# Kernel optimization log

Hardware: AMD Instinct MI355X
Metric: run time of the kernel (lower is better)

## Reference

```python
import jax, jax.numpy as jnp
from jax import lax
import numpy as np

B, C, H, W, D = 8, 128, 96, 96, 4  # D must equal 64//16 = 4 (one UAG per depth slice)


def setup_inputs() -> dict:
    key = jax.random.key(0)
    ks = jax.random.split(key, 9)
    s = 0.5 / np.sqrt(C)  # keep the recurrence numerically stable
    def w(k):
        return jax.random.normal(k, (D, C, C), jnp.float32) * s
    def b(k):
        return jax.random.normal(k, (D, C), jnp.float32) * 0.01
    return {
        "x": jax.random.normal(ks[0], (B, C, H, W, D), jnp.float32),
        "W1": w(ks[1]), "b1": b(ks[2]),  # conv1 per-dag weights/bias (kernel_size=1 -> [C,C])
        "W2": w(ks[3]), "b2": b(ks[4]),  # conv2
        "W4": w(ks[5]), "b4": b(ks[6]),  # conv4
        "W5": w(ks[7]), "b5": b(ks[8]),  # conv5
    }


def _dag(xs, w1, bb1, w2, bb2, w4, bb4, w5, bb5):
    # xs: [B,C,H,W]; one UAG_RNN_4Neigh forward.
    def lin(w, bb, v):  # 1x1 Conv1d == channel matmul; v: [B,C,L]
        return jnp.einsum('oc,bcl->bol', w, v) + bb[None, :, None]

    # --- row recurrence (top -> bottom); row 0 passes through unchanged ---
    def row_step(prev, row):
        new = jax.nn.relu(lin(w1, bb1, row) + lin(w2, bb2, prev))
        return new, new

    row0 = xs[:, :, 0, :]                       # [B,C,W]
    rows = jnp.moveaxis(xs[:, :, 1:, :], 2, 0)  # [H-1,B,C,W]
    _, out_rows = lax.scan(row_step, row0, rows)
    hs = jnp.concatenate([row0[None], out_rows], axis=0)  # [H,B,C,W]
    hs = jnp.moveaxis(hs, 0, 2)                            # [B,C,H,W]

    # --- col recurrence (left -> right); col 0 gets relu only ---
    def col_step(prev, col):
        new = jax.nn.relu(lin(w4, bb4, col) + lin(w5, bb5, prev))
        return new, new

    col0 = jax.nn.relu(hs[:, :, :, 0])           # [B,C,H]
    cols = jnp.moveaxis(hs[:, :, :, 1:], 3, 0)   # [W-1,B,C,H]
    _, out_cols = lax.scan(col_step, col0, cols)
    hse = jnp.concatenate([col0[None], out_cols], axis=0)  # [W,B,C,H]
    return jnp.moveaxis(hse, 0, 3)                           # [B,C,H,W]


def reference(x, W1, b1, W2, b2, W4, b4, W5, b5):
    # vmap over the D=4 depth slices, each with its own dag parameters
    hid = jax.vmap(_dag, in_axes=(-1, 0, 0, 0, 0, 0, 0, 0, 0), out_axes=-1)(
        x, W1, b1, W2, b2, W4, b4, W5, b5)
    return x + hid
```

## Files before the change

kernel.cpp:

```cpp
#include <hip/hip_runtime.h>


typedef short bf16x8 __attribute__((ext_vector_type(8)));
typedef float f32x4 __attribute__((ext_vector_type(4)));
typedef unsigned int uint4v __attribute__((ext_vector_type(4)));

__device__ __forceinline__ unsigned short f2bf(float f) {
  unsigned int u = __builtin_bit_cast(unsigned int, f);
  u = (u + 0x7FFFu + ((u >> 16) & 1u)) >> 16;
  return (unsigned short)u;
}
__device__ __forceinline__ float bf2f(unsigned short h) {
  unsigned int u = ((unsigned int)h) << 16;
  return __builtin_bit_cast(float, u);
}

__device__ __forceinline__ int sigma_k(int kap) {
  int kt = kap >> 5, q = (kap >> 3) & 3, j = kap & 7;
  return kt * 32 + ((j >> 2) << 4) + q * 4 + (j & 3);
}

__global__ __launch_bounds__(256) void prep_kernel(
    const float* __restrict__ W1, const float* __restrict__ b1,
    const float* __restrict__ W2, const float* __restrict__ b2,
    const float* __restrict__ W4, const float* __restrict__ b4,
    const float* __restrict__ W5, const float* __restrict__ b5,
    unsigned short* __restrict__ Wb, float* __restrict__ bs12,
    float* __restrict__ bs45) {
  int gid = blockIdx.x * 256 + threadIdx.x;
  if (gid < 4 * 65536) {
    int m = gid >> 16;
    int r = gid & 65535;
    int kap = r & 127;
    int c = sigma_k(kap);
    const float* src = (m == 0) ? W1 : (m == 1) ? W2 : (m == 2) ? W4 : W5;
    Wb[m * 65536 + r] = f2bf(src[(r >> 7) * 128 + c]);
  } else if (gid < 4 * 65536 + 512) {
    int r = gid - 4 * 65536;
    bs12[r] = b1[r] + b2[r];
  } else if (gid < 4 * 65536 + 1024) {
    int r = gid - 4 * 65536 - 512;
    bs45[r] = b4[r] + b5[r];
  }
}

__global__ __launch_bounds__(256) void transpose_kernel(
    const float* __restrict__ x, unsigned short* __restrict__ act) {
  __shared__ unsigned short tile[128 * 208];
  int bid = blockIdx.x;
  int half = bid & 1;
  int rest = bid >> 1;
  int h = rest % 96;
  int b = rest / 96;
  int wd0 = half * 192;
  int tid = threadIdx.x;
#pragma unroll
  for (int it = 0; it < 12; ++it) {
    int cid = it * 256 + tid;
    int c = cid / 24;
    int k = cid % 24;
    const float* xp = x + ((size_t)(b * 128 + c) * 96 + h) * 384 + wd0 + k * 8;
    float4 v0 = *(const float4*)xp;
    float4 v1 = *(const float4*)(xp + 4);
    bf16x8 pk;
    pk[0] = (short)f2bf(v0.x); pk[1] = (short)f2bf(v0.y);
    pk[2] = (short)f2bf(v0.z); pk[3] = (short)f2bf(v0.w);
    pk[4] = (short)f2bf(v1.x); pk[5] = (short)f2bf(v1.y);
    pk[6] = (short)f2bf(v1.z); pk[7] = (short)f2bf(v1.w);
    int ks = k ^ ((c >> 3) & 7);
    *(bf16x8*)&tile[c * 208 + ks * 8] = pk;
  }
  __syncthreads();
#pragma unroll
  for (int it = 0; it < 12; ++it) {
    int sid = it * 256 + tid;
    int wdl = sid >> 4;
    int cc = sid & 15;
    int k = wdl >> 3, off = wdl & 7;
    int ktq = cc >> 2, qq = cc & 3;
    bf16x8 pk;
#pragma unroll
    for (int j = 0; j < 8; ++j) {
      int c = ktq * 32 + ((j >> 2) << 4) + qq * 4 + (j & 3);
      int ks = k ^ ((c >> 3) & 7);
      pk[j] = (short)tile[c * 208 + ks * 8 + off];
    }
    int wdg = wd0 + wdl;
    int d = wdg & 3, w = wdg >> 2;
    *(bf16x8*)(act + ((((size_t)(b * 4 + d) * 96 + h) * 96 + w) * 128 + cc * 8)) = pk;
  }
}

__global__ __launch_bounds__(128) void row_kernel(
    unsigned short* act, const unsigned short* __restrict__ Wb,
    const float* __restrict__ bs12) {
  __shared__ float slots[4][8][64][4];
  __shared__ int flags[64];
  int bid = blockIdx.x;
  int wt = bid % 6;
  int bd = bid / 6;
  int d = bd & 3;
  int w0 = wt * 16;
  int tid = threadIdx.x;
  int wave = tid >> 6;
  int lane = tid & 63;
  int q = lane >> 4;
  int n = lane & 15;
  volatile int* fprod = &flags[0];
  volatile int* fcons = &flags[32];
  if (tid < 2) flags[tid * 32] = 0;
  __syncthreads();

  size_t bd9216 = (size_t)bd * 9216;
  size_t base = (bd9216 + (size_t)(w0 + n)) * 128 + q * 8;

  if (wave == 1) {
    const unsigned short* w1p = Wb + d * 16384;
    bf16x8 A1[8][4];
#pragma unroll
    for (int mi = 0; mi < 8; ++mi) {
      int c = mi * 16 + n;
#pragma unroll
      for (int kt = 0; kt < 4; ++kt)
        A1[mi][kt] = *(const bf16x8*)(w1p + c * 128 + kt * 32 + q * 8);
    }
    f32x4 bias[8];
#pragma unroll
    for (int mi = 0; mi < 8; ++mi)
#pragma unroll
      for (int r = 0; r < 4; ++r)
        bias[mi][r] = bs12[d * 128 + mi * 16 + q * 4 + r];
    const unsigned short* xrow = act + base;
    bf16x8 Bn[4], Bf[4];
#pragma unroll
    for (int kt = 0; kt < 4; ++kt) {
      Bn[kt] = *(const bf16x8*)(xrow + (size_t)1 * 12288 + kt * 32);
      Bf[kt] = *(const bf16x8*)(xrow + (size_t)2 * 12288 + kt * 32);
    }
#pragma unroll 1
    for (int h = 1; h <= 95; ++h) {
      while (h - *fcons > 3) __builtin_amdgcn_s_sleep(1);
      asm volatile("" ::: "memory");
      f32x4 acc[8];
#pragma unroll
      for (int mi = 0; mi < 8; ++mi)
        acc[mi] = __builtin_amdgcn_mfma_f32_16x16x32_bf16(A1[mi][0], Bn[0],
                                                          bias[mi], 0, 0, 0);
#pragma unroll
      for (int kt = 1; kt < 4; ++kt)
#pragma unroll
        for (int mi = 0; mi < 8; ++mi)
          acc[mi] = __builtin_amdgcn_mfma_f32_16x16x32_bf16(A1[mi][kt], Bn[kt],
                                                            acc[mi], 0, 0, 0);
      int hp = (h + 2 <= 95) ? h + 2 : 95;
      const unsigned short* pf = xrow + (size_t)hp * 12288;
#pragma unroll
      for (int kt = 0; kt < 4; ++kt) {
        Bn[kt] = Bf[kt];
        Bf[kt] = *(const bf16x8*)(pf + kt * 32);
      }
      float* sp = &slots[h & 3][0][lane][0];
#pragma unroll
      for (int mi = 0; mi < 8; ++mi)
        *(f32x4*)(sp + mi * 256) = acc[mi];
      asm volatile("s_waitcnt lgkmcnt(0)" ::: "memory");
      if (lane == 0) *fprod = h;
    }
  } else {
    const unsigned short* w2p = Wb + 65536 + d * 16384;
    bf16x8 A2[8][4];
#pragma unroll
    for (int mi = 0; mi < 8; ++mi) {
      int c = mi * 16 + n;
#pragma unroll
      for (int kt = 0; kt < 4; ++kt)
        A2[mi][kt] = *(const bf16x8*)(w2p + c * 128 + kt * 32 + q * 8);
    }
    const unsigned short* xrow = act + base;
    unsigned short* outrow = act + base + 12288;
    bf16x8 Bp[4];
#pragma unroll
    for (int kt = 0; kt < 4; ++kt)
      Bp[kt] = *(const bf16x8*)(xrow + kt * 32);
#pragma unroll 1
    for (int h = 1; h <= 95; ++h) {
      while (*fprod < h) __builtin_amdgcn_s_sleep(1);
      asm volatile("" ::: "memory");
      const float* sp = &slots[h & 3][0][lane][0];
      f32x4 acc[8];
#pragma unroll
      for (int mi = 0; mi < 8; ++mi)
        acc[mi] = *(const f32x4*)(sp + mi * 256);
#pragma unroll
      for (int kt = 0; kt < 4; ++kt)
#pragma unroll
        for (int mi = 0; mi < 8; ++mi)
          acc[mi] = __builtin_amdgcn_mfma_f32_16x16x32_bf16(A2[mi][kt], Bp[kt],
                                                            acc[mi], 0, 0, 0);
#pragma unroll
      for (int kt = 0; kt < 4; ++kt) {
        unsigned int u0, u1, u2, u3;
        float a0 = fmaxf(acc[2 * kt][0], 0.f);
        float a1 = fmaxf(acc[2 * kt][1], 0.f);
        float a2 = fmaxf(acc[2 * kt][2], 0.f);
        float a3 = fmaxf(acc[2 * kt][3], 0.f);
        float c0 = fmaxf(acc[2 * kt + 1][0], 0.f);
        float c1 = fmaxf(acc[2 * kt + 1][1], 0.f);
        float c2 = fmaxf(acc[2 * kt + 1][2], 0.f);
        float c3 = fmaxf(acc[2 * kt + 1][3], 0.f);
        asm("v_cvt_pk_bf16_f32 %0, %1, %2" : "=v"(u0) : "v"(a0), "v"(a1));
        asm("v_cvt_pk_bf16_f32 %0, %1, %2" : "=v"(u1) : "v"(a2), "v"(a3));
        asm("v_cvt_pk_bf16_f32 %0, %1, %2" : "=v"(u2) : "v"(c0), "v"(c1));
        asm("v_cvt_pk_bf16_f32 %0, %1, %2" : "=v"(u3) : "v"(c2), "v"(c3));
        uint4v uu;
        uu[0] = u0; uu[1] = u1; uu[2] = u2; uu[3] = u3;
        Bp[kt] = __builtin_bit_cast(bf16x8, uu);
        *(bf16x8*)(outrow + kt * 32) = Bp[kt];
      }
      outrow += 12288;
      asm volatile("" ::: "memory");
      if (lane == 0) *fcons = h;
    }
  }
}

__global__ __launch_bounds__(128) void col_kernel(
    unsigned short* act, const unsigned short* __restrict__ Wb,
    const float* __restrict__ bs45) {
  __shared__ float slots[4][8][64][4];
  __shared__ int flags[64];
  int bid = blockIdx.x;
  int ht = bid % 6;
  int bd = bid / 6;
  int d = bd & 3;
  int h0 = ht * 16;
  int tid = threadIdx.x;
  int wave = tid >> 6;
  int lane = tid & 63;
  int q = lane >> 4;
  int n = lane & 15;
  volatile int* fprod = &flags[0];
  volatile int* fcons = &flags[32];
  if (tid < 2) flags[tid * 32] = 0;
  __syncthreads();

  size_t bd9216 = (size_t)bd * 9216;
  size_t base = (bd9216 + (size_t)(h0 + n) * 96) * 128 + q * 8;

  if (wave == 1) {
    const unsigned short* w4p = Wb + 2 * 65536 + d * 16384;
    bf16x8 A1[8][4];
#pragma unroll
    for (int mi = 0; mi < 8; ++mi) {
      int c = mi * 16 + n;
#pragma unroll
      for (int kt = 0; kt < 4; ++kt)
        A1[mi][kt] = *(const bf16x8*)(w4p + c * 128 + kt * 32 + q * 8);
    }
    f32x4 bias[8];
#pragma unroll
    for (int mi = 0; mi < 8; ++mi)
#pragma unroll
      for (int r = 0; r < 4; ++r)
        bias[mi][r] = bs45[d * 128 + mi * 16 + q * 4 + r];
    const unsigned short* ccol = act + base;
    bf16x8 Bn[4], Bf[4];
#pragma unroll
    for (int kt = 0; kt < 4; ++kt) {
      Bn[kt] = *(const bf16x8*)(ccol + (size_t)1 * 128 + kt * 32);
      Bf[kt] = *(const bf16x8*)(ccol + (size_t)2 * 128 + kt * 32);
    }
#pragma unroll 1
    for (int w = 1; w <= 95; ++w) {
      while (w - *fcons > 3) __builtin_amdgcn_s_sleep(1);
      asm volatile("" ::: "memory");
      f32x4 acc[8];
#pragma unroll
      for (int mi = 0; mi < 8; ++mi)
        acc[mi] = __builtin_amdgcn_mfma_f32_16x16x32_bf16(A1[mi][0], Bn[0],
                                                          bias[mi], 0, 0, 0);
#pragma unroll
      for (int kt = 1; kt < 4; ++kt)
#pragma unroll
        for (int mi = 0; mi < 8; ++mi)
          acc[mi] = __builtin_amdgcn_mfma_f32_16x16x32_bf16(A1[mi][kt], Bn[kt],
                                                            acc[mi], 0, 0, 0);
      int wp = (w + 2 <= 95) ? w + 2 : 95;
      const unsigned short* pf = ccol + (size_t)wp * 128;
#pragma unroll
      for (int kt = 0; kt < 4; ++kt) {
        Bn[kt] = Bf[kt];
        Bf[kt] = *(const bf16x8*)(pf + kt * 32);
      }
      float* sp = &slots[w & 3][0][lane][0];
#pragma unroll
      for (int mi = 0; mi < 8; ++mi)
        *(f32x4*)(sp + mi * 256) = acc[mi];
      asm volatile("s_waitcnt lgkmcnt(0)" ::: "memory");
      if (lane == 0) *fprod = w;
    }
  } else {
    const unsigned short* w5p = Wb + 3 * 65536 + d * 16384;
    bf16x8 A2[8][4];
#pragma unroll
    for (int mi = 0; mi < 8; ++mi) {
      int c = mi * 16 + n;
#pragma unroll
      for (int kt = 0; kt < 4; ++kt)
        A2[mi][kt] = *(const bf16x8*)(w5p + c * 128 + kt * 32 + q * 8);
    }
    const unsigned short* ccol = act + base;
    unsigned short* outrow = act + base;
    bf16x8 Bp[4];
#pragma unroll
    for (int kt = 0; kt < 4; ++kt) {
      bf16x8 v = *(const bf16x8*)(ccol + kt * 32);
#pragma unroll
      for (int j = 0; j < 8; ++j) {
        unsigned short uv = (unsigned short)v[j];
        if (uv & 0x8000u) v[j] = 0;
      }
      Bp[kt] = v;
      *(bf16x8*)(outrow + kt * 32) = v;
    }
    outrow += 128;
#pragma unroll 1
    for (int w = 1; w <= 95; ++w) {
      while (*fprod < w) __builtin_amdgcn_s_sleep(1);
      asm volatile("" ::: "memory");
      const float* sp = &slots[w & 3][0][lane][0];
      f32x4 acc[8];
#pragma unroll
      for (int mi = 0; mi < 8; ++mi)
        acc[mi] = *(const f32x4*)(sp + mi * 256);
#pragma unroll
      for (int kt = 0; kt < 4; ++kt)
#pragma unroll
        for (int mi = 0; mi < 8; ++mi)
          acc[mi] = __builtin_amdgcn_mfma_f32_16x16x32_bf16(A2[mi][kt], Bp[kt],
                                                            acc[mi], 0, 0, 0);
#pragma unroll
      for (int kt = 0; kt < 4; ++kt) {
        unsigned int u0, u1, u2, u3;
        float a0 = fmaxf(acc[2 * kt][0], 0.f);
        float a1 = fmaxf(acc[2 * kt][1], 0.f);
        float a2 = fmaxf(acc[2 * kt][2], 0.f);
        float a3 = fmaxf(acc[2 * kt][3], 0.f);
        float c0 = fmaxf(acc[2 * kt + 1][0], 0.f);
        float c1 = fmaxf(acc[2 * kt + 1][1], 0.f);
        float c2 = fmaxf(acc[2 * kt + 1][2], 0.f);
        float c3 = fmaxf(acc[2 * kt + 1][3], 0.f);
        asm("v_cvt_pk_bf16_f32 %0, %1, %2" : "=v"(u0) : "v"(a0), "v"(a1));
        asm("v_cvt_pk_bf16_f32 %0, %1, %2" : "=v"(u1) : "v"(a2), "v"(a3));
        asm("v_cvt_pk_bf16_f32 %0, %1, %2" : "=v"(u2) : "v"(c0), "v"(c1));
        asm("v_cvt_pk_bf16_f32 %0, %1, %2" : "=v"(u3) : "v"(c2), "v"(c3));
        uint4v uu;
        uu[0] = u0; uu[1] = u1; uu[2] = u2; uu[3] = u3;
        Bp[kt] = __builtin_bit_cast(bf16x8, uu);
        *(bf16x8*)(outrow + kt * 32) = Bp[kt];
      }
      outrow += 128;
      asm volatile("" ::: "memory");
      if (lane == 0) *fcons = w;
    }
  }
}

__global__ __launch_bounds__(256) void out_kernel(
    const float* __restrict__ x, const unsigned short* __restrict__ act,
    float* __restrict__ out) {
  __shared__ unsigned short tile[128 * 208];
  int bid = blockIdx.x;
  int half = bid & 1;
  int rest = bid >> 1;
  int h = rest % 96;
  int b = rest / 96;
  int wd0 = half * 192;
  int tid = threadIdx.x;
#pragma unroll
  for (int it = 0; it < 12; ++it) {
    int gid = it * 256 + tid;
    int wdl = gid >> 4;
    int cc = gid & 15;
    int wdg = wd0 + wdl;
    int d = wdg & 3, w = wdg >> 2;
    bf16x8 v = *(const bf16x8*)(
        act + ((((size_t)(b * 4 + d) * 96 + h) * 96 + w) * 128 + cc * 8));
    int k = wdl >> 3, off = wdl & 7;
    int ktq = cc >> 2, qq = cc & 3;
#pragma unroll
    for (int j = 0; j < 8; ++j) {
      int c = ktq * 32 + ((j >> 2) << 4) + qq * 4 + (j & 3);
      int ks = k ^ ((c >> 3) & 7);
      tile[c * 208 + ks * 8 + off] = (unsigned short)v[j];
    }
  }
  __syncthreads();
#pragma unroll
  for (int it = 0; it < 12; ++it) {
    int sid = it * 256 + tid;
    int c = sid / 24;
    int k = sid % 24;
    int ks = k ^ ((c >> 3) & 7);
    bf16x8 pk = *(const bf16x8*)&tile[c * 208 + ks * 8];
    size_t o = ((size_t)(b * 128 + c) * 96 + h) * 384 + wd0 + k * 8;
    float4 a0 = *(const float4*)(x + o);
    float4 a1 = *(const float4*)(x + o + 4);
    float4 r0, r1;
    r0.x = a0.x + bf2f((unsigned short)pk[0]);
    r0.y = a0.y + bf2f((unsigned short)pk[1]);
    r0.z = a0.z + bf2f((unsigned short)pk[2]);
    r0.w = a0.w + bf2f((unsigned short)pk[3]);
    r1.x = a1.x + bf2f((unsigned short)pk[4]);
    r1.y = a1.y + bf2f((unsigned short)pk[5]);
    r1.z = a1.z + bf2f((unsigned short)pk[6]);
    r1.w = a1.w + bf2f((unsigned short)pk[7]);
    *(float4*)(out + o) = r0;
    *(float4*)(out + o + 4) = r1;
  }
}

extern "C" void kernel_launch(void* const* d_in, const int* in_sizes, int n_in,
                              void* d_out, int out_size, void* d_ws,
                              size_t ws_size, hipStream_t stream) {
  (void)in_sizes; (void)n_in; (void)out_size; (void)ws_size;
  const float* x  = (const float*)d_in[0];
  const float* W1 = (const float*)d_in[1];
  const float* b1 = (const float*)d_in[2];
  const float* W2 = (const float*)d_in[3];
  const float* b2 = (const float*)d_in[4];
  const float* W4 = (const float*)d_in[5];
  const float* b4 = (const float*)d_in[6];
  const float* W5 = (const float*)d_in[7];
  const float* b5 = (const float*)d_in[8];
  float* out = (float*)d_out;

  char* ws = (char*)d_ws;
  unsigned short* Wb  = (unsigned short*)(ws);
  float* bs12         = (float*)(ws + 524288);
  float* bs45         = (float*)(ws + 526336);
  unsigned short* act = (unsigned short*)(ws + 528384);

  prep_kernel<<<(4 * 65536 + 1024 + 255) / 256, 256, 0, stream>>>(
      W1, b1, W2, b2, W4, b4, W5, b5, Wb, bs12, bs45);
  transpose_kernel<<<8 * 96 * 2, 256, 0, stream>>>(x, act);
  row_kernel<<<192, 128, 0, stream>>>(act, Wb, bs12);
  col_kernel<<<192, 128, 0, stream>>>(act, Wb, bs45);
  out_kernel<<<8 * 96 * 2, 256, 0, stream>>>(x, act, out);
}
```

Before: 474.8 us.

## Pack four recurrence chains per workgroup and shrink slot ring to two

The row and column recurrence kernels now run four independent 2-wave producer/consumer chains inside one 512-thread workgroup, launching 48 blocks instead of 192. Each chain keeps its own flags and a slot ring in shared memory. The ring is cut from four entries to two, and the producer lookahead is tightened to match so the total shared memory still fits. The aim is to interleave several latency-bound serial chains on the same compute unit to hide MFMA and LDS latency. The trade-off is that only 48 CUs are used and waves on the same SIMD share its matrix unit, with less slack between producer and consumer.

```diff
diff --git a/kernel.cpp b/kernel.cpp
--- a/kernel.cpp
+++ b/kernel.cpp
@@ -91,24 +91,26 @@
   }
 }
 
-__global__ __launch_bounds__(128) void row_kernel(
+__global__ __launch_bounds__(512) void row_kernel(
     unsigned short* act, const unsigned short* __restrict__ Wb,
     const float* __restrict__ bs12) {
-  __shared__ float slots[4][8][64][4];
-  __shared__ int flags[64];
-  int bid = blockIdx.x;
-  int wt = bid % 6;
-  int bd = bid / 6;
+  __shared__ float slots[4][2][8][64][4];
+  __shared__ int flags[4][64];
+  int tid = threadIdx.x;
+  int sc = tid >> 7;
+  int ltid = tid & 127;
+  int wave = ltid >> 6;
+  int lane = ltid & 63;
+  int q = lane >> 4;
+  int n = lane & 15;
+  int cid = blockIdx.x * 4 + sc;
+  int wt = cid % 6;
+  int bd = cid / 6;
   int d = bd & 3;
   int w0 = wt * 16;
-  int tid = threadIdx.x;
-  int wave = tid >> 6;
-  int lane = tid & 63;
-  int q = lane >> 4;
-  int n = lane & 15;
-  volatile int* fprod = &flags[0];
-  volatile int* fcons = &flags[32];
-  if (tid < 2) flags[tid * 32] = 0;
+  volatile int* fprod = &flags[sc][0];
+  volatile int* fcons = &flags[sc][32];
+  if (ltid < 2) flags[sc][ltid * 32] = 0;
   __syncthreads();
 
   size_t bd9216 = (size_t)bd * 9216;
@@ -139,7 +141,7 @@
     }
 #pragma unroll 1
     for (int h = 1; h <= 95; ++h) {
-      while (h - *fcons > 3) __builtin_amdgcn_s_sleep(1);
+      while (h - *fcons > 2) __builtin_amdgcn_s_sleep(1);
       asm volatile("" ::: "memory");
       f32x4 acc[8];
 #pragma unroll
@@ -159,7 +161,7 @@
         Bn[kt] = Bf[kt];
         Bf[kt] = *(const bf16x8*)(pf + kt * 32);
       }
-      float* sp = &slots[h & 3][0][lane][0];
+      float* sp = &slots[sc][h & 1][0][lane][0];
 #pragma unroll
       for (int mi = 0; mi < 8; ++mi)
         *(f32x4*)(sp + mi * 256) = acc[mi];
@@ -186,7 +188,7 @@
     for (int h = 1; h <= 95; ++h) {
       while (*fprod < h) __builtin_amdgcn_s_sleep(1);
       asm volatile("" ::: "memory");
-      const float* sp = &slots[h & 3][0][lane][0];
+      const float* sp = &slots[sc][h & 1][0][lane][0];
       f32x4 acc[8];
 #pragma unroll
       for (int mi = 0; mi < 8; ++mi)
@@ -224,24 +226,26 @@
   }
 }
 
-__global__ __launch_bounds__(128) void col_kernel(
+__global__ __launch_bounds__(512) void col_kernel(
     unsigned short* act, const unsigned short* __restrict__ Wb,
     const float* __restrict__ bs45) {
-  __shared__ float slots[4][8][64][4];
-  __shared__ int flags[64];
-  int bid = blockIdx.x;
-  int ht = bid % 6;
-  int bd = bid / 6;
+  __shared__ float slots[4][2][8][64][4];
+  __shared__ int flags[4][64];
+  int tid = threadIdx.x;
+  int sc = tid >> 7;
+  int ltid = tid & 127;
+  int wave = ltid >> 6;
+  int lane = ltid & 63;
+  int q = lane >> 4;
+  int n = lane & 15;
+  int cid = blockIdx.x * 4 + sc;
+  int ht = cid % 6;
+  int bd = cid / 6;
   int d = bd & 3;
   int h0 = ht * 16;
-  int tid = threadIdx.x;
-  int wave = tid >> 6;
-  int lane = tid & 63;
-  int q = lane >> 4;
-  int n = lane & 15;
-  volatile int* fprod = &flags[0];
-  volatile int* fcons = &flags[32];
-  if (tid < 2) flags[tid * 32] = 0;
+  volatile int* fprod = &flags[sc][0];
+  volatile int* fcons = &flags[sc][32];
+  if (ltid < 2) flags[sc][ltid * 32] = 0;
   __syncthreads();
 
   size_t bd9216 = (size_t)bd * 9216;
@@ -272,7 +276,7 @@
     }
 #pragma unroll 1
     for (int w = 1; w <= 95; ++w) {
-      while (w - *fcons > 3) __builtin_amdgcn_s_sleep(1);
+      while (w - *fcons > 2) __builtin_amdgcn_s_sleep(1);
       asm volatile("" ::: "memory");
       f32x4 acc[8];
 #pragma unroll
@@ -292,7 +296,7 @@
         Bn[kt] = Bf[kt];
         Bf[kt] = *(const bf16x8*)(pf + kt * 32);
       }
-      float* sp = &slots[w & 3][0][lane][0];
+      float* sp = &slots[sc][w & 1][0][lane][0];
 #pragma unroll
       for (int mi = 0; mi < 8; ++mi)
         *(f32x4*)(sp + mi * 256) = acc[mi];
@@ -328,7 +332,7 @@
     for (int w = 1; w <= 95; ++w) {
       while (*fprod < w) __builtin_amdgcn_s_sleep(1);
       asm volatile("" ::: "memory");
-      const float* sp = &slots[w & 3][0][lane][0];
+      const float* sp = &slots[sc][w & 1][0][lane][0];
       f32x4 acc[8];
 #pragma unroll
       for (int mi = 0; mi < 8; ++mi)
@@ -444,7 +448,7 @@
   prep_kernel<<<(4 * 65536 + 1024 + 255) / 256, 256, 0, stream>>>(
       W1, b1, W2, b2, W4, b4, W5, b5, Wb, bs12, bs45);
   transpose_kernel<<<8 * 96 * 2, 256, 0, stream>>>(x, act);
-  row_kernel<<<192, 128, 0, stream>>>(act, Wb, bs12);
-  col_kernel<<<192, 128, 0, stream>>>(act, Wb, bs45);
+  row_kernel<<<48, 512, 0, stream>>>(act, Wb, bs12);
+  col_kernel<<<48, 512, 0, stream>>>(act, Wb, bs45);
   out_kernel<<<8 * 96 * 2, 256, 0, stream>>>(x, act, out);
 }
```

Result: slower. 521.3 us (+9.8%).
